# Kernel optimization log

Hardware: AMD Instinct MI355X
Metric: run time of the kernel (lower is better)

Reference implementation:

```python
import jax, jax.numpy as jnp
import numpy as np

B, T, IMG = 64, 20, 64
IN_DIM = IMG * IMG          # 4096, from x.view(B,-1,64*64)
C_IN = 8                    # input_channels
R_DIM = C_IN * 1024         # 8192, reshape(B,20,-1,32,32) constraint
NF = 64                     # num_filters
Z_DIM = 256
LIN_IN = 2 * NF * 7 * 7     # 6272


def setup_inputs() -> dict:
    key = jax.random.key(0)
    ks = jax.random.split(key, 10)
    x = jax.random.normal(ks[0], (B, T, IMG, IMG), jnp.float32)
    Win = jax.random.normal(ks[1], (IN_DIM, R_DIM), jnp.float32) / np.sqrt(IN_DIM).astype(np.float32)
    U = jax.random.normal(ks[2], (IN_DIM, R_DIM), jnp.float32) / np.sqrt(IN_DIM).astype(np.float32)
    Wr = jax.random.normal(ks[3], (R_DIM, R_DIM), jnp.float32) / np.sqrt(R_DIM).astype(np.float32)
    conv1_w = jax.random.normal(ks[4], (NF, C_IN, 3, 3, 3), jnp.float32) * 0.05
    conv1_b = jax.random.normal(ks[5], (NF,), jnp.float32) * 0.01
    conv2_w = jax.random.normal(ks[6], (2 * NF, NF, 3, 4, 4), jnp.float32) * 0.05
    conv2_b = jax.random.normal(ks[7], (2 * NF,), jnp.float32) * 0.01
    lin_w = jax.random.normal(ks[8], (Z_DIM, LIN_IN), jnp.float32) * 0.02
    lin_b = jax.random.normal(ks[9], (Z_DIM,), jnp.float32) * 0.01
    return {"x": x, "Win": Win, "U": U, "Wr": Wr,
            "conv1_w": conv1_w, "conv1_b": conv1_b,
            "conv2_w": conv2_w, "conv2_b": conv2_b,
            "lin_w": lin_w, "lin_b": lin_b}


def reference(x, Win, U, Wr, conv1_w, conv1_b, conv2_w, conv2_b, lin_w, lin_b):
    Bn = x.shape[0]
    xf = x.reshape(Bn, T, IN_DIM)                      # (B,T,4096)
    h0 = jnp.tanh(xf[:, 0] @ Win)                      # (B,R)
    xU = jnp.einsum('bti,ir->tbr', xf[:, 1:], U)       # precompute input drive (T-1,B,R)

    def step(h, xu):
        h = jnp.tanh(xu + h @ Wr)
        return h, h

    _, hs = jax.lax.scan(step, h0, xU)                 # (T-1,B,R)
    H = jnp.concatenate([h0[None], hs], axis=0)        # (T,B,R)
    H = jnp.swapaxes(H, 0, 1)                          # (B,T,R)

    h = H.reshape(Bn, T, C_IN, 32, 32).transpose(0, 2, 1, 3, 4)  # (B,C,T,32,32)
    dn = ('NCDHW', 'OIDHW', 'NCDHW')
    y = jax.lax.conv_general_dilated(h, conv1_w, (1, 2, 2),
                                     [(1, 1), (1, 1), (1, 1)], dimension_numbers=dn)
    y = y + conv1_b[None, :, None, None, None]
    y = jax.nn.leaky_relu(y, 0.01)                     # (B,NF,20,16,16)
    y = jax.lax.conv_general_dilated(y, conv2_w, (1, 2, 2),
                                     [(1, 1), (0, 0), (0, 0)], dimension_numbers=dn)
    y = y + conv2_b[None, :, None, None, None]
    y = jax.nn.leaky_relu(y, 0.01)                     # (B,2NF,20,7,7)

    y = y.reshape(Bn, -1, T, LIN_IN)                   # (B,1,20,6272), same row-major view as torch
    y = y @ lin_w.T + lin_b                            # (B,1,20,Z_DIM)
    mu, log_var = jnp.split(y, 2, axis=3)
    return mu, log_var
```

## Files before the change

### kernel.cpp

```cpp
#include <hip/hip_runtime.h>

typedef __bf16 v8bf __attribute__((ext_vector_type(8)));
typedef float  v4f  __attribute__((ext_vector_type(4)));
typedef unsigned short us8 __attribute__((ext_vector_type(8)));

__device__ __forceinline__ float bf2f(unsigned short u) {
    union { unsigned int i; float f; } v; v.i = ((unsigned int)u) << 16; return v.f;
}
__device__ __forceinline__ unsigned short f2bf(float f) {
    union { float f; unsigned int i; } v; v.f = f;
    return (unsigned short)((v.i + 0x7fffu + ((v.i >> 16) & 1u)) >> 16);
}

__global__ __launch_bounds__(256)
void transpose_f32_bf16(const float* __restrict__ src,
                        unsigned short* __restrict__ dst, int K, int N)
{
    __shared__ unsigned short tile[64][72];
    const int tid = threadIdx.x;
    const int c0 = blockIdx.x * 64, r0 = blockIdx.y * 64;
    const int tr = tid >> 2, tc4 = tid & 3;
    const float* sp = src + (size_t)(r0 + tr) * N + c0 + tc4 * 16;
#pragma unroll
    for (int j = 0; j < 4; ++j) {
        v4f f = *reinterpret_cast<const v4f*>(sp + j * 4);
#pragma unroll
        for (int e = 0; e < 4; ++e) tile[tr][tc4 * 16 + j * 4 + e] = f2bf(f[e]);
    }
    __syncthreads();
    const int ow = tid >> 3, och = tid & 7;
#pragma unroll
    for (int p = 0; p < 2; ++p) {
        int orow = p * 32 + ow;
        us8 o;
#pragma unroll
        for (int e = 0; e < 8; ++e) o[e] = tile[och * 8 + e][orow];
        *reinterpret_cast<us8*>(dst + (size_t)(c0 + orow) * K + r0 + och * 8) = o;
    }
}

template<int BN, bool STORE_BF16, bool AF32, bool BF32>
__global__ __launch_bounds__(256, 2)
void gemm_bt(const void* __restrict__ Ap, int lda_lo, int lda_hi,
             const void* __restrict__ BTp, int ldb,
             void* __restrict__ Cout, int ldc,
             int ksub, long long csplit_stride)
{
    constexpr int FN  = BN / 32;
    constexpr int BCH = BN / 32;
    const int tid = threadIdx.x;
    const int lane = tid & 63, wid = tid >> 6;
    const int wr = wid >> 1, wc = wid & 1;
    const int nt = blockIdx.x, mt = blockIdx.y, kz = blockIdx.z;
    const int n0 = nt * BN;
    const int kstart = kz * ksub;

    __shared__ unsigned short smem[(64 + BN) * 64];
    char* As = reinterpret_cast<char*>(smem);
    char* Bs = reinterpret_cast<char*>(smem + 64 * 64);

    const unsigned short* A16 = (const unsigned short*)Ap;
    const float*          A32 = (const float*)Ap;
    const unsigned short* B16 = (const unsigned short*)BTp;
    const float*          B32 = (const float*)BTp;

    const int arow = AF32 ? (tid >> 2) : (tid >> 3);
    const int aq   = AF32 ? (tid & 3) : (tid & 7);
    const float* Ab32 = A32 + (size_t)arow * lda_lo + (size_t)mt * lda_hi + kstart + aq * 16;
    const unsigned short* Ab16 = A16 + (size_t)arow * lda_lo + (size_t)mt * lda_hi + kstart + aq * 8;
    const int brow = tid >> 3, bq = tid & 7;
    const float* Bb32 = B32 + (size_t)(n0 + brow) * ldb + kstart + bq * 8;
    const unsigned short* Bb16 = B16 + (size_t)(n0 + brow) * ldb + kstart + bq * 8;

    v4f fa[4];
    us8 ra[2];
    v4f fb[BCH][2];
    us8 rb[BCH];

    auto load = [&](int kk) {
        if (AF32) {
#pragma unroll
            for (int j = 0; j < 4; ++j)
                fa[j] = *reinterpret_cast<const v4f*>(Ab32 + kk + j * 4);
        } else {
#pragma unroll
            for (int p = 0; p < 2; ++p)
                ra[p] = *reinterpret_cast<const us8*>(Ab16 + (size_t)(p * 32) * lda_lo + kk);
        }
        if (BF32) {
#pragma unroll
            for (int p = 0; p < BCH; ++p) {
                fb[p][0] = *reinterpret_cast<const v4f*>(Bb32 + (size_t)(p * 32) * ldb + kk);
                fb[p][1] = *reinterpret_cast<const v4f*>(Bb32 + (size_t)(p * 32) * ldb + kk + 4);
            }
        } else {
#pragma unroll
            for (int p = 0; p < BCH; ++p)
                rb[p] = *reinterpret_cast<const us8*>(Bb16 + (size_t)(p * 32) * ldb + kk);
        }
    };
    auto stage = [&]() {
        if (AF32) {
#pragma unroll
            for (int h = 0; h < 2; ++h) {
                us8 v;
#pragma unroll
                for (int e = 0; e < 8; ++e) v[e] = f2bf(fa[h * 2 + (e >> 2)][e & 3]);
                *reinterpret_cast<us8*>(As + arow * 128 + (((aq * 2 + h) * 16) ^ ((arow & 7) << 4))) = v;
            }
        } else {
#pragma unroll
            for (int p = 0; p < 2; ++p)
                *reinterpret_cast<us8*>(As + (arow + p * 32) * 128 + ((aq * 16) ^ ((arow & 7) << 4))) = ra[p];
        }
#pragma unroll
        for (int p = 0; p < BCH; ++p) {
            us8 v;
            if (BF32) {
#pragma unroll
                for (int e = 0; e < 8; ++e) v[e] = f2bf(fb[p][e >> 2][e & 3]);
            } else v = rb[p];
            *reinterpret_cast<us8*>(Bs + (brow + p * 32) * 128 + ((bq * 16) ^ ((brow & 7) << 4))) = v;
        }
    };

    v4f z4 = {0.f, 0.f, 0.f, 0.f};
    v4f acc[2][FN];
#pragma unroll
    for (int i = 0; i < 2; ++i)
#pragma unroll
        for (int j = 0; j < FN; ++j) acc[i][j] = z4;

    const int l15 = lane & 15, l4 = lane >> 4;
    const int nk = ksub / 64;
    load(0);
    for (int it = 0; it < nk; ++it) {
        __syncthreads();
        stage();
        __syncthreads();
        if (it + 1 < nk) load((it + 1) * 64);
#pragma unroll
        for (int ks = 0; ks < 2; ++ks) {
            const int kb = (ks * 32 + l4 * 8) * 2;
            v8bf af[2], bfr[FN];
#pragma unroll
            for (int fm = 0; fm < 2; ++fm) {
                int row = wr * 32 + fm * 16 + l15;
                af[fm] = *reinterpret_cast<const v8bf*>(As + row * 128 + (kb ^ ((row & 7) << 4)));
            }
#pragma unroll
            for (int fn = 0; fn < FN; ++fn) {
                int row = wc * (BN / 2) + fn * 16 + l15;
                bfr[fn] = *reinterpret_cast<const v8bf*>(Bs + row * 128 + (kb ^ ((row & 7) << 4)));
            }
#pragma unroll
            for (int fm = 0; fm < 2; ++fm)
#pragma unroll
                for (int fn = 0; fn < FN; ++fn)
                    acc[fm][fn] = __builtin_amdgcn_mfma_f32_16x16x32_bf16(af[fm], bfr[fn], acc[fm][fn], 0, 0, 0);
        }
    }
    const long long m0 = (long long)mt * 64;
#pragma unroll
    for (int fm = 0; fm < 2; ++fm)
#pragma unroll
        for (int fn = 0; fn < FN; ++fn)
#pragma unroll
            for (int r = 0; r < 4; ++r) {
                long long row = m0 + wr * 32 + fm * 16 + l4 * 4 + r;
                long long col = n0 + wc * (BN / 2) + fn * 16 + l15;
                long long idx = (long long)kz * csplit_stride + row * ldc + col;
                if (STORE_BF16) reinterpret_cast<unsigned short*>(Cout)[idx] = f2bf(acc[fm][fn][r]);
                else            reinterpret_cast<float*>(Cout)[idx]          = acc[fm][fn][r];
            }
}

__global__ __launch_bounds__(256)
void scan_combine(const float* __restrict__ part, int nparts,
                  const unsigned short* __restrict__ xu,
                  unsigned short* __restrict__ hcur,
                  unsigned short* __restrict__ Hbf, int t)
{
    int i = blockIdx.x * 256 + threadIdx.x;
    float pre = xu ? bf2f(xu[i]) : 0.f;
    for (int z = 0; z < nparts; ++z) pre += part[(size_t)z * 524288 + i];
    float h = tanhf(pre);
    unsigned short hb = f2bf(h);
    hcur[i] = hb;
    int b = i >> 13, r = i & 8191;
    int c = r >> 10, pp = r & 1023;
    Hbf[(((size_t)b * 8 + c) * 20 + t) * 1024 + pp] = hb;
}

__global__ __launch_bounds__(256, 1)
void conv1_kernel(const unsigned short* __restrict__ H,
                  const float* __restrict__ w,
                  const float* __restrict__ bias,
                  unsigned short* __restrict__ y1)
{
    const int b = blockIdx.x, t = blockIdx.y;
    const int tid = threadIdx.x, lane = tid & 63, wid = tid >> 6;
    __shared__ unsigned short in_s[24 * 34 * 34];
    __shared__ unsigned short w_s[64 * 320];

    for (int i = tid; i < 24 * 34 * 34; i += 256) in_s[i] = 0;
    __syncthreads();
    for (int idx = tid; idx < 3072; idx += 256) {
        int g = idx >> 7, rem = idx & 127;
        int iy = rem >> 2, c8 = rem & 3;
        int cc = g / 3, dt = g % 3;
        int ts = t + dt - 1;
        if (ts >= 0 && ts < 20) {
            us8 v = *reinterpret_cast<const us8*>(H + (((size_t)b * 8 + cc) * 20 + ts) * 1024 + iy * 32 + c8 * 8);
            int base = g * 1156 + (iy + 1) * 34 + 1 + c8 * 8;
#pragma unroll
            for (int e = 0; e < 8; ++e) in_s[base + e] = v[e];
        }
    }
    for (int idx = tid; idx < 64 * 288; idx += 256) {
        int n = idx / 288, k = idx % 288;
        int g = k / 12, rm = k % 12, dy = rm >> 2, dx = rm & 3;
        unsigned short val = 0;
        if (dx < 3) {
            int cc = g / 3, dt = g % 3;
            val = f2bf(w[(((n * 8 + cc) * 3 + dt) * 3 + dy) * 3 + dx]);
        }
        *reinterpret_cast<unsigned short*>(reinterpret_cast<char*>(w_s) + n * 640 + ((2 * k) ^ ((n & 7) << 4))) = val;
    }
    __syncthreads();

    v4f z4 = {0.f, 0.f, 0.f, 0.f};
    v4f acc[4][4];
#pragma unroll
    for (int i = 0; i < 4; ++i)
#pragma unroll
        for (int j = 0; j < 4; ++j) acc[i][j] = z4;
    const int l15 = lane & 15, l4 = lane >> 4;

#pragma unroll
    for (int ks = 0; ks < 9; ++ks) {
        v8bf aw[4];
#pragma unroll
        for (int fc = 0; fc < 4; ++fc) {
            int row = fc * 16 + l15;
            aw[fc] = *reinterpret_cast<const v8bf*>(reinterpret_cast<const char*>(w_s)
                       + row * 640 + (((ks * 32 + l4 * 8) * 2) ^ ((row & 7) << 4)));
        }
        v8bf bp[4];
#pragma unroll
        for (int fm = 0; fm < 4; ++fm) {
            int m = wid * 64 + fm * 16 + l15;
            int py = m >> 4, px = m & 15;
            int k0 = ks * 32 + l4 * 8;
            union { v8bf v; unsigned int u[4]; } F;
#pragma unroll
            for (int h = 0; h < 2; ++h) {
                int c = k0 + h * 4;
                int g = c / 12, rm2 = c % 12, dy = rm2 >> 2;
                const char* p = reinterpret_cast<const char*>(in_s)
                                + 2 * (g * 1156 + (2 * py + dy) * 34 + 2 * px);
                F.u[h * 2 + 0] = *reinterpret_cast<const unsigned int*>(p);
                F.u[h * 2 + 1] = *reinterpret_cast<const unsigned int*>(p + 4);
            }
            bp[fm] = F.v;
        }
#pragma unroll
        for (int fc = 0; fc < 4; ++fc)
#pragma unroll
            for (int fm = 0; fm < 4; ++fm)
                acc[fc][fm] = __builtin_amdgcn_mfma_f32_16x16x32_bf16(aw[fc], bp[fm], acc[fc][fm], 0, 0, 0);
    }
#pragma unroll
    for (int fc = 0; fc < 4; ++fc)
#pragma unroll
        for (int fm = 0; fm < 4; ++fm)
#pragma unroll
            for (int r = 0; r < 4; ++r) {
                int co = fc * 16 + l4 * 4 + r;
                int m  = wid * 64 + fm * 16 + l15;
                float v = acc[fc][fm][r] + bias[co];
                v = v > 0.f ? v : 0.01f * v;
                y1[(((size_t)b * 64 + co) * 20 + t) * 256 + m] = f2bf(v);
            }
}

__global__ __launch_bounds__(256, 1)
void conv2_kernel(const unsigned short* __restrict__ y1,
                  const float* __restrict__ w,
                  const float* __restrict__ bias,
                  unsigned short* __restrict__ y2)
{
    const int b = blockIdx.x, t = blockIdx.y;
    const int tid = threadIdx.x, lane = tid & 63, wid = tid >> 6;
    const int wr = wid >> 1, wc = wid & 1;
    __shared__ unsigned short in_s[64 * 768];
    __shared__ unsigned short w_s[128 * 64];

    for (int idx = tid; idx < 6144; idx += 256) {
        int ci = idx / 96, rem = idx % 96;
        int dt = rem / 32, r2 = rem % 32;
        int iy = r2 >> 1, c8 = r2 & 1;
        int ts = t + dt - 1;
        us8 v = {0, 0, 0, 0, 0, 0, 0, 0};
        if (ts >= 0 && ts < 20)
            v = *reinterpret_cast<const us8*>(y1 + (((size_t)b * 64 + ci) * 20 + ts) * 256 + iy * 16 + c8 * 8);
        *reinterpret_cast<us8*>(&in_s[ci * 768 + dt * 256 + iy * 16 + c8 * 8]) = v;
    }

    v4f z4 = {0.f, 0.f, 0.f, 0.f};
    v4f acc[4][2];
#pragma unroll
    for (int i = 0; i < 4; ++i)
#pragma unroll
        for (int j = 0; j < 2; ++j) acc[i][j] = z4;
    const int l15 = lane & 15, l4 = lane >> 4;
    const int wsrow = tid >> 3, wsch = tid & 7;

    for (int kc = 0; kc < 48; ++kc) {
        __syncthreads();
#pragma unroll
        for (int p = 0; p < 4; ++p) {
            int row = p * 32 + wsrow;
            const float* wp = w + (size_t)row * 3072 + kc * 64 + wsch * 8;
            v4f f0 = *reinterpret_cast<const v4f*>(wp);
            v4f f1 = *reinterpret_cast<const v4f*>(wp + 4);
            us8 v;
#pragma unroll
            for (int e = 0; e < 8; ++e) v[e] = f2bf(e < 4 ? f0[e] : f1[e - 4]);
            *reinterpret_cast<us8*>(reinterpret_cast<char*>(w_s) + row * 128 + ((wsch * 16) ^ ((row & 7) << 4))) = v;
        }
        __syncthreads();
#pragma unroll
        for (int ks = 0; ks < 2; ++ks) {
            int klocal = ks * 32 + l4 * 8;
            v8bf aw[4];
#pragma unroll
            for (int fc = 0; fc < 4; ++fc) {
                int row = wc * 64 + fc * 16 + l15;
                aw[fc] = *reinterpret_cast<const v8bf*>(reinterpret_cast<const char*>(w_s)
                           + row * 128 + ((klocal * 2) ^ ((row & 7) << 4)));
            }
            v8bf bp[2];
#pragma unroll
            for (int fm = 0; fm < 2; ++fm) {
                int m = wr * 32 + fm * 16 + l15;
                m = m < 49 ? m : 48;
                int py = m / 7, px = m - py * 7;
                union { v8bf v; unsigned int u[4]; } F;
#pragma unroll
                for (int h = 0; h < 2; ++h) {
                    int c = kc * 64 + klocal + h * 4;
                    int ci = c / 48, rc = c % 48;
                    int dt = rc >> 4, dy = (rc >> 2) & 3;
                    const char* p = reinterpret_cast<const char*>(in_s)
                                    + 2 * (ci * 768 + dt * 256 + (2 * py + dy) * 16 + 2 * px);
                    F.u[h * 2 + 0] = *reinterpret_cast<const unsigned int*>(p);
                    F.u[h * 2 + 1] = *reinterpret_cast<const unsigned int*>(p + 4);
                }
                bp[fm] = F.v;
            }
#pragma unroll
            for (int fc = 0; fc < 4; ++fc)
#pragma unroll
                for (int fm = 0; fm < 2; ++fm)
                    acc[fc][fm] = __builtin_amdgcn_mfma_f32_16x16x32_bf16(aw[fc], bp[fm], acc[fc][fm], 0, 0, 0);
        }
    }
#pragma unroll
    for (int fc = 0; fc < 4; ++fc)
#pragma unroll
        for (int fm = 0; fm < 2; ++fm)
#pragma unroll
            for (int r = 0; r < 4; ++r) {
                int m = wr * 32 + fm * 16 + l15;
                if (m < 49) {
                    int co = wc * 64 + fc * 16 + l4 * 4 + r;
                    float v = acc[fc][fm][r] + bias[co];
                    v = v > 0.f ? v : 0.01f * v;
                    y2[(((size_t)b * 128 + co) * 20 + t) * 49 + m] = f2bf(v);
                }
            }
}

__global__ __launch_bounds__(256)
void lin_epi(const float* __restrict__ linC, const float* __restrict__ lb,
             float* __restrict__ out)
{
    int i = blockIdx.x * 256 + threadIdx.x;
    int m = i >> 8, n = i & 255;
    float v = linC[i] + lb[n];
    size_t o = (n < 128) ? ((size_t)m * 128 + n) : (163840 + (size_t)m * 128 + (n - 128));
    out[o] = v;
}

extern "C" void kernel_launch(void* const* d_in, const int* in_sizes, int n_in,
                              void* d_out, int out_size, void* d_ws, size_t ws_size,
                              hipStream_t stream)
{
    const float* x   = (const float*)d_in[0];
    const float* Win = (const float*)d_in[1];
    const float* U   = (const float*)d_in[2];
    const float* Wr  = (const float*)d_in[3];
    const float* c1w = (const float*)d_in[4];
    const float* c1b = (const float*)d_in[5];
    const float* c2w = (const float*)d_in[6];
    const float* c2b = (const float*)d_in[7];
    const float* lw  = (const float*)d_in[8];
    const float* lb  = (const float*)d_in[9];

    char* ws = (char*)d_ws;
    unsigned short* WrT  = (unsigned short*)(ws);
    unsigned short* WT   = (unsigned short*)(ws + 134217728ll);
    unsigned short* y1   = (unsigned short*)(ws + 134217728ll);
    unsigned short* y2   = (unsigned short*)(ws + 176160768ll);
    unsigned short* XALL = (unsigned short*)(ws + 201326592ll);
    unsigned short* Hbf  = (unsigned short*)(ws + 222298112ll);
    float*          part = (float*)        (ws + 243269632ll);
    unsigned short* hcur = (unsigned short*)(ws + 251658240ll);
    float*          linC = (float*)        (ws + 252706816ll);
    float*          out  = (float*)d_out;

    transpose_f32_bf16<<<dim3(128, 64), 256, 0, stream>>>(Win, WT, 4096, 8192);
    gemm_bt<128, false, true, false><<<dim3(64, 1, 4), 256, 0, stream>>>(
        x, 81920, 0, WT, 4096, part, 8192, 1024, 524288ll);
    scan_combine<<<2048, 256, 0, stream>>>(part, 4, (const unsigned short*)nullptr, hcur, Hbf, 0);

    transpose_f32_bf16<<<dim3(128, 64), 256, 0, stream>>>(U, WT, 4096, 8192);
    gemm_bt<128, true, true, false><<<dim3(64, 19, 1), 256, 0, stream>>>(
        x + 4096, 81920, 4096, WT, 4096, XALL + 524288, 8192, 4096, 0ll);

    transpose_f32_bf16<<<dim3(128, 128), 256, 0, stream>>>(Wr, WrT, 8192, 8192);
    for (int t = 1; t < 20; ++t) {
        gemm_bt<64, false, false, false><<<dim3(128, 1, 4), 256, 0, stream>>>(
            hcur, 8192, 0, WrT, 8192, part, 8192, 2048, 524288ll);
        scan_combine<<<2048, 256, 0, stream>>>(part, 4, XALL + (size_t)t * 524288, hcur, Hbf, t);
    }

    conv1_kernel<<<dim3(64, 20), 256, 0, stream>>>(Hbf, c1w, c1b, y1);
    conv2_kernel<<<dim3(64, 20), 256, 0, stream>>>(y1, c2w, c2b, y2);

    gemm_bt<128, false, false, true><<<dim3(2, 20, 1), 256, 0, stream>>>(
        y2, 6272, 6272 * 64, lw, 6272, linC, 256, 6272, 0ll);
    lin_epi<<<1280, 256, 0, stream>>>(linC, lb, out);
}
```

Measured before the change: 1.463 ms.

## Fuse recurrence GEMM with tanh, channel-last conv layouts, pre-converted weights, split-K linear

Replaces the split-K recurrent GEMM plus separate combine kernel with one fused kernel per step. Each block covers a 32-column slice over the full K and applies the tanh epilogue directly, using ping-pong hidden buffers. Conv weights are now converted to bf16 once up front, and H and y1 are stored channel-last so both convs load contiguous 16-byte im2col vectors. conv2 also moves to 512 threads with larger K chunks. The final linear GEMM gains a 7-way split-K, reduced in the epilogue. The aim is fewer launches, less partial-sum traffic and fewer scalar LDS gathers, at the cost of only 256 blocks per recurrence step, which may underfill the GPU.

```diff
diff --git a/kernel.cpp b/kernel.cpp
--- a/kernel.cpp
+++ b/kernel.cpp
@@ -11,6 +11,7 @@
     union { float f; unsigned int i; } v; v.f = f;
     return (unsigned short)((v.i + 0x7fffu + ((v.i >> 16) & 1u)) >> 16);
 }
+__device__ __forceinline__ int sw(int b) { return b ^ (((b >> 7) & 7) << 4); }
 
 __global__ __launch_bounds__(256)
 void transpose_f32_bf16(const float* __restrict__ src,
@@ -175,206 +176,288 @@
             }
 }
 
+template<bool AF32>
+__global__ __launch_bounds__(256, 2)
+void scan_fused(const void* __restrict__ Ap, int lda,
+                const unsigned short* __restrict__ BT, int ldb, int K,
+                const unsigned short* __restrict__ xu,
+                unsigned short* __restrict__ hnext,
+                unsigned short* __restrict__ Hbf, int t)
+{
+    const int tid = threadIdx.x, lane = tid & 63, wid = tid >> 6;
+    const int wr = wid >> 1, wc = wid & 1;
+    const int n0 = blockIdx.x * 32;
+
+    __shared__ unsigned short smem[96 * 64];
+    char* As = reinterpret_cast<char*>(smem);
+    char* Bs = reinterpret_cast<char*>(smem + 64 * 64);
+
+    const float*          A32 = (const float*)Ap;
+    const unsigned short* A16 = (const unsigned short*)Ap;
+    const int arow = AF32 ? (tid >> 2) : (tid >> 3);
+    const int aq   = AF32 ? (tid & 3) : (tid & 7);
+    const float* Ab32 = A32 + (size_t)arow * lda + aq * 16;
+    const unsigned short* Ab16 = A16 + (size_t)arow * lda + aq * 8;
+    const int brow = tid >> 3, bq = tid & 7;
+    const unsigned short* Bb = BT + (size_t)(n0 + brow) * ldb + bq * 8;
+
+    v4f fa[4];
+    us8 ra[2], rb;
+    auto load = [&](int kk) {
+        if (AF32) {
+#pragma unroll
+            for (int j = 0; j < 4; ++j)
+                fa[j] = *reinterpret_cast<const v4f*>(Ab32 + kk + j * 4);
+        } else {
+#pragma unroll
+            for (int p = 0; p < 2; ++p)
+                ra[p] = *reinterpret_cast<const us8*>(Ab16 + (size_t)(p * 32) * lda + kk);
+        }
+        rb = *reinterpret_cast<const us8*>(Bb + kk);
+    };
+    auto stage = [&]() {
+        if (AF32) {
+#pragma unroll
+            for (int h = 0; h < 2; ++h) {
+                us8 v;
+#pragma unroll
+                for (int e = 0; e < 8; ++e) v[e] = f2bf(fa[h * 2 + (e >> 2)][e & 3]);
+                *reinterpret_cast<us8*>(As + arow * 128 + (((aq * 2 + h) * 16) ^ ((arow & 7) << 4))) = v;
+            }
+        } else {
+#pragma unroll
+            for (int p = 0; p < 2; ++p)
+                *reinterpret_cast<us8*>(As + (arow + p * 32) * 128 + ((aq * 16) ^ ((arow & 7) << 4))) = ra[p];
+        }
+        *reinterpret_cast<us8*>(Bs + brow * 128 + ((bq * 16) ^ ((brow & 7) << 4))) = rb;
+    };
+
+    v4f z4 = {0.f, 0.f, 0.f, 0.f};
+    v4f acc[2];
+    acc[0] = z4; acc[1] = z4;
+    const int l15 = lane & 15, l4 = lane >> 4;
+    const int nk = K / 64;
+    load(0);
+    for (int it = 0; it < nk; ++it) {
+        __syncthreads();
+        stage();
+        __syncthreads();
+        if (it + 1 < nk) load((it + 1) * 64);
+#pragma unroll
+        for (int ks = 0; ks < 2; ++ks) {
+            const int kb = (ks * 32 + l4 * 8) * 2;
+            v8bf af[2], bfr;
+#pragma unroll
+            for (int fm = 0; fm < 2; ++fm) {
+                int row = wr * 32 + fm * 16 + l15;
+                af[fm] = *reinterpret_cast<const v8bf*>(As + row * 128 + (kb ^ ((row & 7) << 4)));
+            }
+            {
+                int row = wc * 16 + l15;
+                bfr = *reinterpret_cast<const v8bf*>(Bs + row * 128 + (kb ^ ((row & 7) << 4)));
+            }
+#pragma unroll
+            for (int fm = 0; fm < 2; ++fm)
+                acc[fm] = __builtin_amdgcn_mfma_f32_16x16x32_bf16(af[fm], bfr, acc[fm], 0, 0, 0);
+        }
+    }
+#pragma unroll
+    for (int fm = 0; fm < 2; ++fm)
+#pragma unroll
+        for (int r = 0; r < 4; ++r) {
+            int row = wr * 32 + fm * 16 + l4 * 4 + r;
+            int col = n0 + wc * 16 + l15;
+            float pre = acc[fm][r];
+            if (xu) pre += bf2f(xu[row * 8192 + col]);
+            unsigned short hb = f2bf(tanhf(pre));
+            hnext[row * 8192 + col] = hb;
+            int c = col >> 10, pp = col & 1023;
+            Hbf[(((size_t)row * 20 + t) * 1024 + pp) * 8 + c] = hb;
+        }
+}
+
 __global__ __launch_bounds__(256)
-void scan_combine(const float* __restrict__ part, int nparts,
-                  const unsigned short* __restrict__ xu,
-                  unsigned short* __restrict__ hcur,
-                  unsigned short* __restrict__ Hbf, int t)
-{
-    int i = blockIdx.x * 256 + threadIdx.x;
-    float pre = xu ? bf2f(xu[i]) : 0.f;
-    for (int z = 0; z < nparts; ++z) pre += part[(size_t)z * 524288 + i];
-    float h = tanhf(pre);
-    unsigned short hb = f2bf(h);
-    hcur[i] = hb;
-    int b = i >> 13, r = i & 8191;
-    int c = r >> 10, pp = r & 1023;
-    Hbf[(((size_t)b * 8 + c) * 20 + t) * 1024 + pp] = hb;
-}
-
-__global__ __launch_bounds__(256, 1)
+void cvt_w1(const float* __restrict__ w, unsigned short* __restrict__ o)
+{
+    int idx = blockIdx.x * 256 + threadIdx.x;
+    if (idx >= 64 * 224) return;
+    int co = idx / 224, k = idx % 224;
+    int g = k >> 3, ci = k & 7;
+    float v = 0.f;
+    if (g < 27) {
+        int dt = g / 9, rr = g % 9, dy = rr / 3, dx = rr % 3;
+        v = w[(((co * 8 + ci) * 3 + dt) * 3 + dy) * 3 + dx];
+    }
+    o[idx] = f2bf(v);
+}
+__global__ __launch_bounds__(256)
+void cvt_w2(const float* __restrict__ w, unsigned short* __restrict__ o)
+{
+    int idx = blockIdx.x * 256 + threadIdx.x;
+    if (idx >= 128 * 3072) return;
+    int co = idx / 3072, k = idx % 3072;
+    int g = k >> 6, ci = k & 63;
+    int dt = g >> 4, dy = (g >> 2) & 3, dx = g & 3;
+    o[idx] = f2bf(w[(((co * 64 + ci) * 3 + dt) * 4 + dy) * 4 + dx]);
+}
+
+__global__ __launch_bounds__(256, 2)
 void conv1_kernel(const unsigned short* __restrict__ H,
-                  const float* __restrict__ w,
+                  const unsigned short* __restrict__ w1,
                   const float* __restrict__ bias,
                   unsigned short* __restrict__ y1)
 {
     const int b = blockIdx.x, t = blockIdx.y;
     const int tid = threadIdx.x, lane = tid & 63, wid = tid >> 6;
-    __shared__ unsigned short in_s[24 * 34 * 34];
-    __shared__ unsigned short w_s[64 * 320];
-
-    for (int i = tid; i < 24 * 34 * 34; i += 256) in_s[i] = 0;
+    __shared__ unsigned short in_s[3 * 33 * 33 * 8];
+    __shared__ unsigned short w_s[64 * 224];
+
+    for (int i = tid; i < 13068; i += 256) reinterpret_cast<unsigned int*>(in_s)[i] = 0;
     __syncthreads();
-    for (int idx = tid; idx < 3072; idx += 256) {
-        int g = idx >> 7, rem = idx & 127;
-        int iy = rem >> 2, c8 = rem & 3;
-        int cc = g / 3, dt = g % 3;
+    for (int idx = tid; idx < 3 * 1024; idx += 256) {
+        int dt = idx >> 10, rem = idx & 1023;
+        int iy = rem >> 5, ix = rem & 31;
         int ts = t + dt - 1;
         if (ts >= 0 && ts < 20) {
-            us8 v = *reinterpret_cast<const us8*>(H + (((size_t)b * 8 + cc) * 20 + ts) * 1024 + iy * 32 + c8 * 8);
-            int base = g * 1156 + (iy + 1) * 34 + 1 + c8 * 8;
-#pragma unroll
-            for (int e = 0; e < 8; ++e) in_s[base + e] = v[e];
-        }
-    }
-    for (int idx = tid; idx < 64 * 288; idx += 256) {
-        int n = idx / 288, k = idx % 288;
-        int g = k / 12, rm = k % 12, dy = rm >> 2, dx = rm & 3;
-        unsigned short val = 0;
-        if (dx < 3) {
-            int cc = g / 3, dt = g % 3;
-            val = f2bf(w[(((n * 8 + cc) * 3 + dt) * 3 + dy) * 3 + dx]);
-        }
-        *reinterpret_cast<unsigned short*>(reinterpret_cast<char*>(w_s) + n * 640 + ((2 * k) ^ ((n & 7) << 4))) = val;
+            us8 v = *reinterpret_cast<const us8*>(H + (((size_t)b * 20 + ts) * 1024 + rem) * 8);
+            int byte = ((dt * 33 + iy + 1) * 33 + (ix + 1)) * 16;
+            *reinterpret_cast<us8*>(reinterpret_cast<char*>(in_s) + sw(byte)) = v;
+        }
+    }
+    for (int idx = tid; idx < 64 * 28; idx += 256) {
+        int co = idx / 28, j = idx % 28;
+        us8 v = *reinterpret_cast<const us8*>(w1 + co * 224 + j * 8);
+        *reinterpret_cast<us8*>(reinterpret_cast<char*>(w_s) + sw(co * 448 + j * 16)) = v;
     }
     __syncthreads();
 
+    const int l15 = lane & 15, l4 = lane >> 4;
+    const int m_lo = wid * 64 + l15;
     v4f z4 = {0.f, 0.f, 0.f, 0.f};
     v4f acc[4][4];
 #pragma unroll
     for (int i = 0; i < 4; ++i)
 #pragma unroll
         for (int j = 0; j < 4; ++j) acc[i][j] = z4;
-    const int l15 = lane & 15, l4 = lane >> 4;
-
-#pragma unroll
-    for (int ks = 0; ks < 9; ++ks) {
-        v8bf aw[4];
+
+#pragma unroll
+    for (int ks = 0; ks < 7; ++ks) {
+        int g = ks * 4 + l4;
+        int gc = g < 27 ? g : 26;
+        int dt = gc / 9, rr = gc % 9, dy = rr / 3, dx = rr % 3;
+        v8bf ap[4], aw[4];
+#pragma unroll
+        for (int fm = 0; fm < 4; ++fm) {
+            int m = fm * 16 + m_lo;
+            int py = m >> 4, px = m & 15;
+            int byte = ((dt * 33 + 2 * py + dy) * 33 + 2 * px + dx) * 16;
+            ap[fm] = *reinterpret_cast<const v8bf*>(reinterpret_cast<const char*>(in_s) + sw(byte));
+        }
+        int kb2 = (ks * 32 + l4 * 8) * 2;
 #pragma unroll
         for (int fc = 0; fc < 4; ++fc) {
-            int row = fc * 16 + l15;
-            aw[fc] = *reinterpret_cast<const v8bf*>(reinterpret_cast<const char*>(w_s)
-                       + row * 640 + (((ks * 32 + l4 * 8) * 2) ^ ((row & 7) << 4)));
-        }
-        v8bf bp[4];
-#pragma unroll
-        for (int fm = 0; fm < 4; ++fm) {
-            int m = wid * 64 + fm * 16 + l15;
-            int py = m >> 4, px = m & 15;
-            int k0 = ks * 32 + l4 * 8;
-            union { v8bf v; unsigned int u[4]; } F;
-#pragma unroll
-            for (int h = 0; h < 2; ++h) {
-                int c = k0 + h * 4;
-                int g = c / 12, rm2 = c % 12, dy = rm2 >> 2;
-                const char* p = reinterpret_cast<const char*>(in_s)
-                                + 2 * (g * 1156 + (2 * py + dy) * 34 + 2 * px);
-                F.u[h * 2 + 0] = *reinterpret_cast<const unsigned int*>(p);
-                F.u[h * 2 + 1] = *reinterpret_cast<const unsigned int*>(p + 4);
-            }
-            bp[fm] = F.v;
-        }
+            int co = fc * 16 + l15;
+            aw[fc] = *reinterpret_cast<const v8bf*>(reinterpret_cast<const char*>(w_s) + sw(co * 448 + kb2));
+        }
+#pragma unroll
+        for (int fm = 0; fm < 4; ++fm)
+#pragma unroll
+            for (int fc = 0; fc < 4; ++fc)
+                acc[fm][fc] = __builtin_amdgcn_mfma_f32_16x16x32_bf16(ap[fm], aw[fc], acc[fm][fc], 0, 0, 0);
+    }
+#pragma unroll
+    for (int fm = 0; fm < 4; ++fm)
 #pragma unroll
         for (int fc = 0; fc < 4; ++fc)
 #pragma unroll
-            for (int fm = 0; fm < 4; ++fm)
-                acc[fc][fm] = __builtin_amdgcn_mfma_f32_16x16x32_bf16(aw[fc], bp[fm], acc[fc][fm], 0, 0, 0);
-    }
-#pragma unroll
-    for (int fc = 0; fc < 4; ++fc)
-#pragma unroll
-        for (int fm = 0; fm < 4; ++fm)
-#pragma unroll
             for (int r = 0; r < 4; ++r) {
-                int co = fc * 16 + l4 * 4 + r;
-                int m  = wid * 64 + fm * 16 + l15;
-                float v = acc[fc][fm][r] + bias[co];
+                int m  = wid * 64 + fm * 16 + l4 * 4 + r;
+                int co = fc * 16 + l15;
+                float v = acc[fm][fc][r] + bias[co];
                 v = v > 0.f ? v : 0.01f * v;
-                y1[(((size_t)b * 64 + co) * 20 + t) * 256 + m] = f2bf(v);
-            }
-}
-
-__global__ __launch_bounds__(256, 1)
+                y1[(((size_t)b * 20 + t) * 256 + m) * 64 + co] = f2bf(v);
+            }
+}
+
+__global__ __launch_bounds__(512, 1)
 void conv2_kernel(const unsigned short* __restrict__ y1,
-                  const float* __restrict__ w,
+                  const unsigned short* __restrict__ w2,
                   const float* __restrict__ bias,
                   unsigned short* __restrict__ y2)
 {
     const int b = blockIdx.x, t = blockIdx.y;
     const int tid = threadIdx.x, lane = tid & 63, wid = tid >> 6;
-    const int wr = wid >> 1, wc = wid & 1;
-    __shared__ unsigned short in_s[64 * 768];
-    __shared__ unsigned short w_s[128 * 64];
-
-    for (int idx = tid; idx < 6144; idx += 256) {
-        int ci = idx / 96, rem = idx % 96;
-        int dt = rem / 32, r2 = rem % 32;
-        int iy = r2 >> 1, c8 = r2 & 1;
+    const int wc = wid >> 1, wr = wid & 1;
+    __shared__ unsigned short in_s[3 * 256 * 64];
+    __shared__ unsigned short w_s[128 * 192];
+
+    for (int idx = tid; idx < 6144; idx += 512) {
+        int dt = idx >> 11, rem = idx & 2047;
+        int slot = rem >> 3, c8 = rem & 7;
         int ts = t + dt - 1;
         us8 v = {0, 0, 0, 0, 0, 0, 0, 0};
         if (ts >= 0 && ts < 20)
-            v = *reinterpret_cast<const us8*>(y1 + (((size_t)b * 64 + ci) * 20 + ts) * 256 + iy * 16 + c8 * 8);
-        *reinterpret_cast<us8*>(&in_s[ci * 768 + dt * 256 + iy * 16 + c8 * 8]) = v;
-    }
+            v = *reinterpret_cast<const us8*>(y1 + (((size_t)b * 20 + ts) * 256 + slot) * 64 + c8 * 8);
+        int byte = (dt * 256 + slot) * 128 + c8 * 16;
+        *reinterpret_cast<us8*>(reinterpret_cast<char*>(in_s) + sw(byte)) = v;
+    }
+
+    const int l15 = lane & 15, l4 = lane >> 4;
+    const int m0v = wr * 32 + l15, m1v = m0v + 16;
+    const int m0c = m0v < 49 ? m0v : 48, m1c = m1v < 49 ? m1v : 48;
+    const int py0 = m0c / 7, px0 = m0c - py0 * 7;
+    const int py1 = m1c / 7, px1 = m1c - py1 * 7;
 
     v4f z4 = {0.f, 0.f, 0.f, 0.f};
-    v4f acc[4][2];
-#pragma unroll
-    for (int i = 0; i < 4; ++i)
+    v4f acc[2][2];
+#pragma unroll
+    for (int i = 0; i < 2; ++i)
 #pragma unroll
         for (int j = 0; j < 2; ++j) acc[i][j] = z4;
-    const int l15 = lane & 15, l4 = lane >> 4;
-    const int wsrow = tid >> 3, wsch = tid & 7;
-
-    for (int kc = 0; kc < 48; ++kc) {
+
+    for (int kc = 0; kc < 16; ++kc) {
         __syncthreads();
-#pragma unroll
-        for (int p = 0; p < 4; ++p) {
-            int row = p * 32 + wsrow;
-            const float* wp = w + (size_t)row * 3072 + kc * 64 + wsch * 8;
-            v4f f0 = *reinterpret_cast<const v4f*>(wp);
-            v4f f1 = *reinterpret_cast<const v4f*>(wp + 4);
-            us8 v;
-#pragma unroll
-            for (int e = 0; e < 8; ++e) v[e] = f2bf(e < 4 ? f0[e] : f1[e - 4]);
-            *reinterpret_cast<us8*>(reinterpret_cast<char*>(w_s) + row * 128 + ((wsch * 16) ^ ((row & 7) << 4))) = v;
+        for (int idx = tid; idx < 3072; idx += 512) {
+            int co = idx / 24, j = idx % 24;
+            us8 v = *reinterpret_cast<const us8*>(w2 + (size_t)co * 3072 + kc * 192 + j * 8);
+            *reinterpret_cast<us8*>(reinterpret_cast<char*>(w_s) + sw(co * 384 + j * 16)) = v;
         }
         __syncthreads();
 #pragma unroll
-        for (int ks = 0; ks < 2; ++ks) {
-            int klocal = ks * 32 + l4 * 8;
-            v8bf aw[4];
-#pragma unroll
-            for (int fc = 0; fc < 4; ++fc) {
-                int row = wc * 64 + fc * 16 + l15;
+        for (int ks = 0; ks < 6; ++ks) {
+            int kb = ks * 32 + l4 * 8;
+            int kabs = kc * 192 + kb;
+            int g = kabs >> 6, ci0 = kabs & 63;
+            int dt = g >> 4, dy = (g >> 2) & 3, dx = g & 3;
+            v8bf aw[2], bp[2];
+#pragma unroll
+            for (int fc = 0; fc < 2; ++fc) {
+                int co = wc * 32 + fc * 16 + l15;
                 aw[fc] = *reinterpret_cast<const v8bf*>(reinterpret_cast<const char*>(w_s)
-                           + row * 128 + ((klocal * 2) ^ ((row & 7) << 4)));
-            }
-            v8bf bp[2];
-#pragma unroll
-            for (int fm = 0; fm < 2; ++fm) {
-                int m = wr * 32 + fm * 16 + l15;
-                m = m < 49 ? m : 48;
-                int py = m / 7, px = m - py * 7;
-                union { v8bf v; unsigned int u[4]; } F;
-#pragma unroll
-                for (int h = 0; h < 2; ++h) {
-                    int c = kc * 64 + klocal + h * 4;
-                    int ci = c / 48, rc = c % 48;
-                    int dt = rc >> 4, dy = (rc >> 2) & 3;
-                    const char* p = reinterpret_cast<const char*>(in_s)
-                                    + 2 * (ci * 768 + dt * 256 + (2 * py + dy) * 16 + 2 * px);
-                    F.u[h * 2 + 0] = *reinterpret_cast<const unsigned int*>(p);
-                    F.u[h * 2 + 1] = *reinterpret_cast<const unsigned int*>(p + 4);
-                }
-                bp[fm] = F.v;
-            }
-#pragma unroll
-            for (int fc = 0; fc < 4; ++fc)
+                           + sw(co * 384 + kb * 2));
+            }
+            {
+                int byte0 = ((dt * 16 + 2 * py0 + dy) * 16 + 2 * px0 + dx) * 128 + ci0 * 2;
+                bp[0] = *reinterpret_cast<const v8bf*>(reinterpret_cast<const char*>(in_s) + sw(byte0));
+                int byte1 = ((dt * 16 + 2 * py1 + dy) * 16 + 2 * px1 + dx) * 128 + ci0 * 2;
+                bp[1] = *reinterpret_cast<const v8bf*>(reinterpret_cast<const char*>(in_s) + sw(byte1));
+            }
+#pragma unroll
+            for (int fc = 0; fc < 2; ++fc)
 #pragma unroll
                 for (int fm = 0; fm < 2; ++fm)
                     acc[fc][fm] = __builtin_amdgcn_mfma_f32_16x16x32_bf16(aw[fc], bp[fm], acc[fc][fm], 0, 0, 0);
         }
     }
 #pragma unroll
-    for (int fc = 0; fc < 4; ++fc)
+    for (int fc = 0; fc < 2; ++fc)
 #pragma unroll
         for (int fm = 0; fm < 2; ++fm)
 #pragma unroll
             for (int r = 0; r < 4; ++r) {
-                int m = wr * 32 + fm * 16 + l15;
+                int co = wc * 32 + fc * 16 + l4 * 4 + r;
+                int m  = wr * 32 + fm * 16 + l15;
                 if (m < 49) {
-                    int co = wc * 64 + fc * 16 + l4 * 4 + r;
                     float v = acc[fc][fm][r] + bias[co];
                     v = v > 0.f ? v : 0.01f * v;
                     y2[(((size_t)b * 128 + co) * 20 + t) * 49 + m] = f2bf(v);
@@ -388,7 +471,9 @@
 {
     int i = blockIdx.x * 256 + threadIdx.x;
     int m = i >> 8, n = i & 255;
-    float v = linC[i] + lb[n];
+    float v = lb[n];
+#pragma unroll
+    for (int z = 0; z < 7; ++z) v += linC[(size_t)z * 327680 + i];
     size_t o = (n < 128) ? ((size_t)m * 128 + n) : (163840 + (size_t)m * 128 + (n - 128));
     out[o] = v;
 }
@@ -415,15 +500,19 @@
     unsigned short* y2   = (unsigned short*)(ws + 176160768ll);
     unsigned short* XALL = (unsigned short*)(ws + 201326592ll);
     unsigned short* Hbf  = (unsigned short*)(ws + 222298112ll);
-    float*          part = (float*)        (ws + 243269632ll);
-    unsigned short* hcur = (unsigned short*)(ws + 251658240ll);
-    float*          linC = (float*)        (ws + 252706816ll);
+    unsigned short* hb0  = (unsigned short*)(ws + 243269632ll);
+    unsigned short* hb1  = (unsigned short*)(ws + 244318208ll);
+    float*          linC = (float*)        (ws + 245366784ll);
+    unsigned short* w1bf = (unsigned short*)(ws + 254541824ll);
+    unsigned short* w2bf = (unsigned short*)(ws + 254570496ll);
     float*          out  = (float*)d_out;
 
+    cvt_w1<<<56, 256, 0, stream>>>(c1w, w1bf);
+    cvt_w2<<<1536, 256, 0, stream>>>(c2w, w2bf);
+
     transpose_f32_bf16<<<dim3(128, 64), 256, 0, stream>>>(Win, WT, 4096, 8192);
-    gemm_bt<128, false, true, false><<<dim3(64, 1, 4), 256, 0, stream>>>(
-        x, 81920, 0, WT, 4096, part, 8192, 1024, 524288ll);
-    scan_combine<<<2048, 256, 0, stream>>>(part, 4, (const unsigned short*)nullptr, hcur, Hbf, 0);
+    scan_fused<true><<<256, 256, 0, stream>>>(x, 81920, WT, 4096, 4096,
+                                              (const unsigned short*)nullptr, hb0, Hbf, 0);
 
     transpose_f32_bf16<<<dim3(128, 64), 256, 0, stream>>>(U, WT, 4096, 8192);
     gemm_bt<128, true, true, false><<<dim3(64, 19, 1), 256, 0, stream>>>(
@@ -431,15 +520,16 @@
 
     transpose_f32_bf16<<<dim3(128, 128), 256, 0, stream>>>(Wr, WrT, 8192, 8192);
     for (int t = 1; t < 20; ++t) {
-        gemm_bt<64, false, false, false><<<dim3(128, 1, 4), 256, 0, stream>>>(
-            hcur, 8192, 0, WrT, 8192, part, 8192, 2048, 524288ll);
-        scan_combine<<<2048, 256, 0, stream>>>(part, 4, XALL + (size_t)t * 524288, hcur, Hbf, t);
-    }
-
-    conv1_kernel<<<dim3(64, 20), 256, 0, stream>>>(Hbf, c1w, c1b, y1);
-    conv2_kernel<<<dim3(64, 20), 256, 0, stream>>>(y1, c2w, c2b, y2);
-
-    gemm_bt<128, false, false, true><<<dim3(2, 20, 1), 256, 0, stream>>>(
-        y2, 6272, 6272 * 64, lw, 6272, linC, 256, 6272, 0ll);
+        unsigned short* hprev = (t & 1) ? hb0 : hb1;
+        unsigned short* hnext = (t & 1) ? hb1 : hb0;
+        scan_fused<false><<<256, 256, 0, stream>>>(hprev, 8192, WrT, 8192, 8192,
+                                                   XALL + (size_t)t * 524288, hnext, Hbf, t);
+    }
+
+    conv1_kernel<<<dim3(64, 20), 256, 0, stream>>>(Hbf, w1bf, c1b, y1);
+    conv2_kernel<<<dim3(64, 20), 512, 0, stream>>>(y1, w2bf, c2b, y2);
+
+    gemm_bt<128, false, false, true><<<dim3(2, 20, 7), 256, 0, stream>>>(
+        y2, 6272, 6272 * 64, lw, 6272, linC, 256, 896, 327680ll);
     lin_epi<<<1280, 256, 0, stream>>>(linC, lb, out);
 }
```

Result: slower. 1.890 ms (+29.2%).
